# Optimization experiments

Hardware: AMD Instinct MI355X
Metric: run time of the kernel (lower is better)

The kernel has to match this reference:

```python
import jax, jax.numpy as jnp
import numpy as np

N_GRAPHS, NODES_PER, DEG, D = 128, 1024, 32, 256
N = N_GRAPHS * NODES_PER          # 131072 nodes
E = N * DEG                       # 4194304 edges
RATIO = 0.8
K = int(np.ceil(RATIO * NODES_PER))  # 820 nodes kept per graph


def setup_inputs() -> dict:
    key = jax.random.key(0)
    k1, k2, k3, k4 = jax.random.split(key, 4)
    x = jax.random.normal(k1, (N, D), dtype=jnp.float32)
    # intra-graph random edges: endpoints within [0, NODES_PER) + graph offset
    src = jax.random.randint(k2, (E,), 0, NODES_PER)
    dst = jax.random.randint(k3, (E,), 0, NODES_PER)
    goff = (jnp.arange(E) // (NODES_PER * DEG)) * NODES_PER
    edge_index = jnp.stack([src + goff, dst + goff]).astype(jnp.int32)
    batch = jnp.repeat(jnp.arange(N_GRAPHS, dtype=jnp.int32), NODES_PER)
    W = jax.random.normal(k4, (D, 1), dtype=jnp.float32) / np.sqrt(D)
    b = jnp.zeros((1,), dtype=jnp.float32)
    return {"x": x, "edge_index": edge_index, "batch": batch, "W": W, "b": b}


def _gcn_score(x, edge_index, W, b):
    # GCNConv(in_channels, 1) with added self-loops and symmetric normalization
    n = x.shape[0]
    row, col = edge_index[0], edge_index[1]  # source, target
    # degree at target, init 1.0 accounts for self-loop
    deg = jnp.ones((n,), x.dtype).at[col].add(jnp.ones_like(col, dtype=x.dtype))
    dinv = jax.lax.rsqrt(deg)
    h = x @ W                                 # [n, 1]
    norm = dinv[row] * dinv[col]              # [E]
    agg = jnp.zeros_like(h).at[col].add(norm[:, None] * h[row])
    agg = agg + (dinv * dinv)[:, None] * h    # self-loop contribution deg^-1 * h_i
    return (agg + b).squeeze(-1)              # [n]


def reference(x, edge_index, batch, W, b):
    score = _gcn_score(x, edge_index, W, b)                     # [N]
    # per-graph top-k (graphs are contiguous, equal size)
    score_g = score.reshape(N_GRAPHS, NODES_PER)
    _, idx = jax.lax.top_k(score_g, K)                          # [G, K]
    perm = (idx + jnp.arange(N_GRAPHS)[:, None] * NODES_PER).reshape(-1)  # [G*K]
    x_new = x[perm] * jnp.tanh(score[perm])[:, None]            # [G*K, D]
    batch_new = batch[perm]
    # filter_adj: remap kept nodes to new ids, mask edges with dropped endpoints
    new_id = jnp.full((x.shape[0],), -1, dtype=perm.dtype).at[perm].set(
        jnp.arange(perm.shape[0], dtype=perm.dtype))
    r2 = new_id[edge_index[0]]
    c2 = new_id[edge_index[1]]
    edge_mask = (r2 >= 0) & (c2 >= 0)                           # [E] valid edges
    edge_index_new = jnp.where(edge_mask, jnp.stack([r2, c2]), -1)  # [2, E], -1 = dropped
    return x_new, edge_index_new, edge_mask, batch_new, perm
```

## Files before the change

kernel.cpp:

```cpp
#include <hip/hip_runtime.h>
#include <math.h>

constexpr int NG    = 128;
constexpr int NP    = 1024;
constexpr int D     = 256;
constexpr int NTOT  = NG * NP;
constexpr int EPG   = NP * 32;
constexpr int ET    = NTOT * 32;
constexpr int KK    = 820;
constexpr int NKEEP = NG * KK;
constexpr int BPG   = 4;
constexpr int EPB   = EPG / BPG;
constexpr int NBE   = NG * BPG;

constexpr int K1_BLOCKS = 2048;
constexpr int K4_BLOCKS = 2048;
constexpr int K1_ROWS_PER_WAVE = NTOT / (K1_BLOCKS * 4);

constexpr long long OUT_X     = 0;
constexpr long long OUT_EI0   = (long long)NKEEP * D;
constexpr long long OUT_EI1   = OUT_EI0 + ET;
constexpr long long OUT_MASK  = OUT_EI0 + 2LL * ET;
constexpr long long OUT_BATCH = OUT_MASK + ET;
constexpr long long OUT_PERM  = OUT_BATCH + NKEEP;

__global__ __launch_bounds__(256) void k1_h_deg(const float* __restrict__ x,
                                                const float* __restrict__ W,
                                                const int* __restrict__ cols,
                                                float* __restrict__ h,
                                                int* __restrict__ new_id,
                                                int* __restrict__ deg_part) {
    __shared__ int cnt[NP];
    const int b    = blockIdx.x;
    const int t    = threadIdx.x;
    const int w    = t >> 6;
    const int lane = t & 63;
    const bool do_deg = (b < NBE);

    if (do_deg) {
        for (int i = t; i < NP; i += 256) cnt[i] = 0;
        __syncthreads();
    }

    float4 w4 = ((const float4*)W)[lane];
    const int base = (b * 4 + w) * K1_ROWS_PER_WAVE;
    for (int r = 0; r < K1_ROWS_PER_WAVE; ++r) {
        const int row = base + r;
        float4 a = ((const float4*)(x + (size_t)row * D))[lane];
        float s = a.x * w4.x + a.y * w4.y + a.z * w4.z + a.w * w4.w;
#pragma unroll
        for (int off = 32; off > 0; off >>= 1) s += __shfl_down(s, off, 64);
        if (lane == 0) { h[row] = s; new_id[row] = -1; }
    }

    if (do_deg) {
        const int g = b >> 2;
        const int4* c4 = (const int4*)(cols + (size_t)g * EPG + (size_t)(b & 3) * EPB);
#pragma unroll
        for (int i = t; i < EPB / 4; i += 256) {
            int4 c = c4[i];
            atomicAdd(&cnt[c.x & (NP - 1)], 1);
            atomicAdd(&cnt[c.y & (NP - 1)], 1);
            atomicAdd(&cnt[c.z & (NP - 1)], 1);
            atomicAdd(&cnt[c.w & (NP - 1)], 1);
        }
        __syncthreads();
        int* dst = deg_part + (size_t)b * NP;
        for (int i = t; i < NP; i += 256) dst[i] = cnt[i];
    }
}

__global__ __launch_bounds__(256) void k2_acc(const int* __restrict__ rows,
                                              const int* __restrict__ cols,
                                              const float* __restrict__ h,
                                              const int* __restrict__ deg_part,
                                              float* __restrict__ acc_part) {
    __shared__ float ul[NP];
    __shared__ float acc[NP];
    const int b = blockIdx.x;
    const int g = b >> 2;
    const int* dp = deg_part + (size_t)g * BPG * NP;
    for (int i = threadIdx.x; i < NP; i += 256) {
        int d = 1 + dp[i] + dp[NP + i] + dp[2 * NP + i] + dp[3 * NP + i];
        ul[i]  = rsqrtf((float)d) * h[g * NP + i];
        acc[i] = 0.0f;
    }
    __syncthreads();
    size_t eoff = (size_t)g * EPG + (size_t)(b & 3) * EPB;
    const int4* c4 = (const int4*)(cols + eoff);
    const int4* r4 = (const int4*)(rows + eoff);
#pragma unroll
    for (int i = threadIdx.x; i < EPB / 4; i += 256) {
        int4 c = c4[i];
        int4 r = r4[i];
        atomicAdd(&acc[c.x & (NP - 1)], ul[r.x & (NP - 1)]);
        atomicAdd(&acc[c.y & (NP - 1)], ul[r.y & (NP - 1)]);
        atomicAdd(&acc[c.z & (NP - 1)], ul[r.z & (NP - 1)]);
        atomicAdd(&acc[c.w & (NP - 1)], ul[r.w & (NP - 1)]);
    }
    __syncthreads();
    float* dst = acc_part + (size_t)b * NP;
    for (int i = threadIdx.x; i < NP; i += 256) dst[i] = acc[i];
}

__global__ __launch_bounds__(1024) void k3_sort(
        const float* __restrict__ h, const float* __restrict__ b,
        const int* __restrict__ deg_part, const float* __restrict__ acc_part,
        int* __restrict__ perm_i, int* __restrict__ new_id,
        float* __restrict__ factor,
        float* __restrict__ out_perm, float* __restrict__ out_batch) {
    __shared__ unsigned long long sk[NP];
    __shared__ float scl[NP];

    const int g = blockIdx.x;
    const int t = threadIdx.x;
    const int*   dp = deg_part + (size_t)g * BPG * NP;
    const float* ap = acc_part + (size_t)g * BPG * NP;

    int   d  = 1 + dp[t] + dp[NP + t] + dp[2 * NP + t] + dp[3 * NP + t];
    float av = ap[t] + ap[NP + t] + ap[2 * NP + t] + ap[3 * NP + t];
    float hv = h[g * NP + t];
    float di = rsqrtf((float)d);
    float score = di * av + di * di * hv + b[0];
    scl[t] = score;

    unsigned int fu = __float_as_uint(score);
    unsigned int s  = (fu & 0x80000000u) ? ~fu : (fu | 0x80000000u);
    unsigned long long key = ((unsigned long long)(~s) << 32) | (unsigned int)t;

    for (int k = 2; k <= NP; k <<= 1) {
        for (int j = k >> 1; j > 0; j >>= 1) {
            unsigned long long other;
            if (j < 64) {
                other = __shfl_xor(key, j, 64);
            } else {
                sk[t] = key;
                __syncthreads();
                other = sk[t ^ j];
                __syncthreads();
            }
            bool take_min = (((t & k) == 0) == ((t & j) == 0));
            bool omin = other < key;
            key = (take_min == omin) ? other : key;
        }
    }

    if (t < KK) {
        int idx  = (int)(key & 0xFFFFFFFFull);
        int node = g * NP + idx;
        int j    = g * KK + t;
        perm_i[j]    = node;
        new_id[node] = j;
        out_perm[j]  = (float)node;
        out_batch[j] = (float)g;
        factor[j]    = tanhf(scl[idx]);
    }
}

__global__ __launch_bounds__(256) void k4_gather_edge(
        const float* __restrict__ x,
        const int* __restrict__ rows, const int* __restrict__ cols,
        const int* __restrict__ new_id,
        const int* __restrict__ perm_i, const float* __restrict__ factor,
        float* __restrict__ out) {
    __shared__ int nid[NP];
    const int b    = blockIdx.x;
    const int t    = threadIdx.x;
    const int w    = t >> 6;
    const int lane = t & 63;

    if (b < NBE) {
        const int g = b >> 2;
        for (int i = t; i < NP; i += 256) nid[i] = new_id[g * NP + i];
        __syncthreads();
        size_t eoff = (size_t)g * EPG + (size_t)(b & 3) * EPB;
        const int4* r4 = (const int4*)(rows + eoff);
        const int4* c4 = (const int4*)(cols + eoff);
        float4* orr = (float4*)(out + OUT_EI0  + eoff);
        float4* occ = (float4*)(out + OUT_EI1  + eoff);
        float4* omm = (float4*)(out + OUT_MASK + eoff);
#pragma unroll
        for (int i = t; i < EPB / 4; i += 256) {
            int4 r = r4[i];
            int4 c = c4[i];
            float4 fr, fc, fm;
            {
                int nr = nid[r.x & (NP - 1)], nc = nid[c.x & (NP - 1)];
                bool m = (nr >= 0) && (nc >= 0);
                fr.x = m ? (float)nr : -1.0f; fc.x = m ? (float)nc : -1.0f; fm.x = m ? 1.0f : 0.0f;
            }
            {
                int nr = nid[r.y & (NP - 1)], nc = nid[c.y & (NP - 1)];
                bool m = (nr >= 0) && (nc >= 0);
                fr.y = m ? (float)nr : -1.0f; fc.y = m ? (float)nc : -1.0f; fm.y = m ? 1.0f : 0.0f;
            }
            {
                int nr = nid[r.z & (NP - 1)], nc = nid[c.z & (NP - 1)];
                bool m = (nr >= 0) && (nc >= 0);
                fr.z = m ? (float)nr : -1.0f; fc.z = m ? (float)nc : -1.0f; fm.z = m ? 1.0f : 0.0f;
            }
            {
                int nr = nid[r.w & (NP - 1)], nc = nid[c.w & (NP - 1)];
                bool m = (nr >= 0) && (nc >= 0);
                fr.w = m ? (float)nr : -1.0f; fc.w = m ? (float)nc : -1.0f; fm.w = m ? 1.0f : 0.0f;
            }
            orr[i] = fr;
            occ[i] = fc;
            omm[i] = fm;
        }
    }

    const int gw = b * 4 + w;
    for (int j = gw; j < NKEEP; j += K4_BLOCKS * 4) {
        const int node = perm_i[j];
        const float f  = factor[j];
        float4 v = ((const float4*)(x + (size_t)node * D))[lane];
        ((float4*)(out + OUT_X + (size_t)j * D))[lane] =
            make_float4(v.x * f, v.y * f, v.z * f, v.w * f);
    }
}

extern "C" void kernel_launch(void* const* d_in, const int* in_sizes, int n_in,
                              void* d_out, int out_size, void* d_ws, size_t ws_size,
                              hipStream_t stream) {
    (void)in_sizes; (void)n_in; (void)out_size; (void)ws_size;

    const float* x  = (const float*)d_in[0];
    const int*   ei = (const int*)d_in[1];
    const float* W  = (const float*)d_in[3];
    const float* b  = (const float*)d_in[4];
    float* out = (float*)d_out;

    float* wsf      = (float*)d_ws;
    float* h        = wsf;
    int*   new_id   = (int*)(wsf + NTOT);
    int*   perm_i   = (int*)(wsf + 2 * NTOT);
    float* factor   = wsf + 2 * NTOT + NKEEP;
    int*   deg_part = (int*)(wsf + 2 * NTOT + 2 * NKEEP);
    float* acc_part = wsf + 2 * NTOT + 2 * NKEEP + NBE * NP;

    const int* rows = ei;
    const int* cols = ei + ET;

    hipLaunchKernelGGL(k1_h_deg, dim3(K1_BLOCKS), dim3(256), 0, stream,
                       x, W, cols, h, new_id, deg_part);
    hipLaunchKernelGGL(k2_acc, dim3(NBE), dim3(256), 0, stream,
                       rows, cols, h, deg_part, acc_part);
    hipLaunchKernelGGL(k3_sort, dim3(NG), dim3(1024), 0, stream,
                       h, b, deg_part, acc_part, perm_i, new_id, factor,
                       out + OUT_PERM, out + OUT_BATCH);
    hipLaunchKernelGGL(k4_gather_edge, dim3(K4_BLOCKS), dim3(256), 0, stream,
                       x, rows, cols, new_id, perm_i, factor, out + OUT_X);
}
```

Baseline: 346.4 us.

## Fuse degree, aggregation and top-k sort into one per-graph kernel

Degree counting, edge aggregation and the bitonic top-k now run in a single 1024-thread block per graph, so the partial degree and accumulator arrays no longer make a round trip through global memory and one launch is dropped. The projection kernel processes 16 rows per wave with four independent reductions in flight. In the gather/edge kernel, edge blocks and row-gather blocks are split, and outputs use nontemporal stores. In exchange, the aggregation phase now runs on only 128 blocks, which may underuse the GPU, and each block reads its graph's edges twice.

```diff
diff --git a/kernel.cpp b/kernel.cpp
--- a/kernel.cpp
+++ b/kernel.cpp
@@ -14,8 +14,9 @@
 constexpr int NBE   = NG * BPG;
 
 constexpr int K1_BLOCKS = 2048;
-constexpr int K4_BLOCKS = 2048;
-constexpr int K1_ROWS_PER_WAVE = NTOT / (K1_BLOCKS * 4);
+constexpr int K3_BLOCKS = 2048;
+
+typedef float v4f __attribute__((ext_vector_type(4)));
 
 constexpr long long OUT_X     = 0;
 constexpr long long OUT_EI0   = (long long)NKEEP * D;
@@ -24,73 +25,83 @@
 constexpr long long OUT_BATCH = OUT_MASK + ET;
 constexpr long long OUT_PERM  = OUT_BATCH + NKEEP;
 
-__global__ __launch_bounds__(256) void k1_h_deg(const float* __restrict__ x,
-                                                const float* __restrict__ W,
-                                                const int* __restrict__ cols,
-                                                float* __restrict__ h,
-                                                int* __restrict__ new_id,
-                                                int* __restrict__ deg_part) {
-    __shared__ int cnt[NP];
-    const int b    = blockIdx.x;
+__global__ __launch_bounds__(256) void k1_h(const float* __restrict__ x,
+                                            const float* __restrict__ W,
+                                            float* __restrict__ h,
+                                            int* __restrict__ new_id) {
     const int t    = threadIdx.x;
     const int w    = t >> 6;
     const int lane = t & 63;
-    const bool do_deg = (b < NBE);
-
-    if (do_deg) {
-        for (int i = t; i < NP; i += 256) cnt[i] = 0;
-        __syncthreads();
-    }
+    const int gw   = blockIdx.x * 4 + w;
 
     float4 w4 = ((const float4*)W)[lane];
-    const int base = (b * 4 + w) * K1_ROWS_PER_WAVE;
-    for (int r = 0; r < K1_ROWS_PER_WAVE; ++r) {
-        const int row = base + r;
-        float4 a = ((const float4*)(x + (size_t)row * D))[lane];
-        float s = a.x * w4.x + a.y * w4.y + a.z * w4.z + a.w * w4.w;
-#pragma unroll
-        for (int off = 32; off > 0; off >>= 1) s += __shfl_down(s, off, 64);
-        if (lane == 0) { h[row] = s; new_id[row] = -1; }
-    }
-
-    if (do_deg) {
-        const int g = b >> 2;
-        const int4* c4 = (const int4*)(cols + (size_t)g * EPG + (size_t)(b & 3) * EPB);
-#pragma unroll
-        for (int i = t; i < EPB / 4; i += 256) {
-            int4 c = c4[i];
-            atomicAdd(&cnt[c.x & (NP - 1)], 1);
-            atomicAdd(&cnt[c.y & (NP - 1)], 1);
-            atomicAdd(&cnt[c.z & (NP - 1)], 1);
-            atomicAdd(&cnt[c.w & (NP - 1)], 1);
-        }
-        __syncthreads();
-        int* dst = deg_part + (size_t)b * NP;
-        for (int i = t; i < NP; i += 256) dst[i] = cnt[i];
-    }
-}
-
-__global__ __launch_bounds__(256) void k2_acc(const int* __restrict__ rows,
-                                              const int* __restrict__ cols,
-                                              const float* __restrict__ h,
-                                              const int* __restrict__ deg_part,
-                                              float* __restrict__ acc_part) {
-    __shared__ float ul[NP];
+    const float4* xp = (const float4*)(x + (size_t)gw * 16 * D);
+
+#pragma unroll
+    for (int c = 0; c < 4; ++c) {
+        float4 a0 = xp[(c * 4 + 0) * 64 + lane];
+        float4 a1 = xp[(c * 4 + 1) * 64 + lane];
+        float4 a2 = xp[(c * 4 + 2) * 64 + lane];
+        float4 a3 = xp[(c * 4 + 3) * 64 + lane];
+        float s0 = a0.x * w4.x + a0.y * w4.y + a0.z * w4.z + a0.w * w4.w;
+        float s1 = a1.x * w4.x + a1.y * w4.y + a1.z * w4.z + a1.w * w4.w;
+        float s2 = a2.x * w4.x + a2.y * w4.y + a2.z * w4.z + a2.w * w4.w;
+        float s3 = a3.x * w4.x + a3.y * w4.y + a3.z * w4.z + a3.w * w4.w;
+#pragma unroll
+        for (int off = 32; off > 0; off >>= 1) {
+            s0 += __shfl_down(s0, off, 64);
+            s1 += __shfl_down(s1, off, 64);
+            s2 += __shfl_down(s2, off, 64);
+            s3 += __shfl_down(s3, off, 64);
+        }
+        if (lane == 0) {
+            const int r = gw * 16 + c * 4;
+            h[r] = s0; h[r + 1] = s1; h[r + 2] = s2; h[r + 3] = s3;
+            new_id[r]     = -1; new_id[r + 1] = -1;
+            new_id[r + 2] = -1; new_id[r + 3] = -1;
+        }
+    }
+}
+
+__global__ __launch_bounds__(1024) void k2_graph(
+        const float* __restrict__ h,  const float* __restrict__ bptr,
+        const int* __restrict__ rows, const int* __restrict__ cols,
+        int* __restrict__ perm_i,     int* __restrict__ new_id,
+        float* __restrict__ factor,
+        float* __restrict__ out_perm, float* __restrict__ out_batch) {
+    __shared__ unsigned long long sk[NP];
     __shared__ float acc[NP];
-    const int b = blockIdx.x;
-    const int g = b >> 2;
-    const int* dp = deg_part + (size_t)g * BPG * NP;
-    for (int i = threadIdx.x; i < NP; i += 256) {
-        int d = 1 + dp[i] + dp[NP + i] + dp[2 * NP + i] + dp[3 * NP + i];
-        ul[i]  = rsqrtf((float)d) * h[g * NP + i];
-        acc[i] = 0.0f;
-    }
-    __syncthreads();
-    size_t eoff = (size_t)g * EPG + (size_t)(b & 3) * EPB;
-    const int4* c4 = (const int4*)(cols + eoff);
-    const int4* r4 = (const int4*)(rows + eoff);
-#pragma unroll
-    for (int i = threadIdx.x; i < EPB / 4; i += 256) {
+    __shared__ float scl[NP];
+    int*   cnt = (int*)sk;
+    float* ul  = (float*)sk + NP;
+
+    const int g = blockIdx.x;
+    const int t = threadIdx.x;
+
+    const float hv = h[g * NP + t];
+    cnt[t] = 0;
+    __syncthreads();
+
+    const int4* c4 = (const int4*)(cols + (size_t)g * EPG);
+    const int4* r4 = (const int4*)(rows + (size_t)g * EPG);
+
+#pragma unroll
+    for (int i = t; i < EPG / 4; i += 1024) {
+        int4 c = c4[i];
+        atomicAdd(&cnt[c.x & (NP - 1)], 1);
+        atomicAdd(&cnt[c.y & (NP - 1)], 1);
+        atomicAdd(&cnt[c.z & (NP - 1)], 1);
+        atomicAdd(&cnt[c.w & (NP - 1)], 1);
+    }
+    __syncthreads();
+
+    const float di = rsqrtf((float)(1 + cnt[t]));
+    ul[t]  = di * hv;
+    acc[t] = 0.0f;
+    __syncthreads();
+
+#pragma unroll
+    for (int i = t; i < EPG / 4; i += 1024) {
         int4 c = c4[i];
         int4 r = r4[i];
         atomicAdd(&acc[c.x & (NP - 1)], ul[r.x & (NP - 1)]);
@@ -99,29 +110,8 @@
         atomicAdd(&acc[c.w & (NP - 1)], ul[r.w & (NP - 1)]);
     }
     __syncthreads();
-    float* dst = acc_part + (size_t)b * NP;
-    for (int i = threadIdx.x; i < NP; i += 256) dst[i] = acc[i];
-}
-
-__global__ __launch_bounds__(1024) void k3_sort(
-        const float* __restrict__ h, const float* __restrict__ b,
-        const int* __restrict__ deg_part, const float* __restrict__ acc_part,
-        int* __restrict__ perm_i, int* __restrict__ new_id,
-        float* __restrict__ factor,
-        float* __restrict__ out_perm, float* __restrict__ out_batch) {
-    __shared__ unsigned long long sk[NP];
-    __shared__ float scl[NP];
-
-    const int g = blockIdx.x;
-    const int t = threadIdx.x;
-    const int*   dp = deg_part + (size_t)g * BPG * NP;
-    const float* ap = acc_part + (size_t)g * BPG * NP;
-
-    int   d  = 1 + dp[t] + dp[NP + t] + dp[2 * NP + t] + dp[3 * NP + t];
-    float av = ap[t] + ap[NP + t] + ap[2 * NP + t] + ap[3 * NP + t];
-    float hv = h[g * NP + t];
-    float di = rsqrtf((float)d);
-    float score = di * av + di * di * hv + b[0];
+
+    const float score = di * acc[t] + di * di * hv + bptr[0];
     scl[t] = score;
 
     unsigned int fu = __float_as_uint(score);
@@ -157,7 +147,7 @@
     }
 }
 
-__global__ __launch_bounds__(256) void k4_gather_edge(
+__global__ __launch_bounds__(256) void k3_gather_edge(
         const float* __restrict__ x,
         const int* __restrict__ rows, const int* __restrict__ cols,
         const int* __restrict__ new_id,
@@ -176,14 +166,14 @@
         size_t eoff = (size_t)g * EPG + (size_t)(b & 3) * EPB;
         const int4* r4 = (const int4*)(rows + eoff);
         const int4* c4 = (const int4*)(cols + eoff);
-        float4* orr = (float4*)(out + OUT_EI0  + eoff);
-        float4* occ = (float4*)(out + OUT_EI1  + eoff);
-        float4* omm = (float4*)(out + OUT_MASK + eoff);
+        v4f* orr = (v4f*)(out + OUT_EI0  + eoff);
+        v4f* occ = (v4f*)(out + OUT_EI1  + eoff);
+        v4f* omm = (v4f*)(out + OUT_MASK + eoff);
 #pragma unroll
         for (int i = t; i < EPB / 4; i += 256) {
             int4 r = r4[i];
             int4 c = c4[i];
-            float4 fr, fc, fm;
+            v4f fr, fc, fm;
             {
                 int nr = nid[r.x & (NP - 1)], nc = nid[c.x & (NP - 1)];
                 bool m = (nr >= 0) && (nc >= 0);
@@ -204,19 +194,20 @@
                 bool m = (nr >= 0) && (nc >= 0);
                 fr.w = m ? (float)nr : -1.0f; fc.w = m ? (float)nc : -1.0f; fm.w = m ? 1.0f : 0.0f;
             }
-            orr[i] = fr;
-            occ[i] = fc;
-            omm[i] = fm;
-        }
-    }
-
-    const int gw = b * 4 + w;
-    for (int j = gw; j < NKEEP; j += K4_BLOCKS * 4) {
-        const int node = perm_i[j];
-        const float f  = factor[j];
-        float4 v = ((const float4*)(x + (size_t)node * D))[lane];
-        ((float4*)(out + OUT_X + (size_t)j * D))[lane] =
-            make_float4(v.x * f, v.y * f, v.z * f, v.w * f);
+            __builtin_nontemporal_store(fr, &orr[i]);
+            __builtin_nontemporal_store(fc, &occ[i]);
+            __builtin_nontemporal_store(fm, &omm[i]);
+        }
+    } else {
+        const int gw = (b - NBE) * 4 + w;
+        for (int j = gw; j < NKEEP; j += (K3_BLOCKS - NBE) * 4) {
+            const int node = perm_i[j];
+            const float f  = factor[j];
+            float4 v = ((const float4*)(x + (size_t)node * D))[lane];
+            v4f o;
+            o.x = v.x * f; o.y = v.y * f; o.z = v.z * f; o.w = v.w * f;
+            __builtin_nontemporal_store(o, &((v4f*)(out + OUT_X + (size_t)j * D))[lane]);
+        }
     }
 }
 
@@ -236,19 +227,15 @@
     int*   new_id   = (int*)(wsf + NTOT);
     int*   perm_i   = (int*)(wsf + 2 * NTOT);
     float* factor   = wsf + 2 * NTOT + NKEEP;
-    int*   deg_part = (int*)(wsf + 2 * NTOT + 2 * NKEEP);
-    float* acc_part = wsf + 2 * NTOT + 2 * NKEEP + NBE * NP;
 
     const int* rows = ei;
     const int* cols = ei + ET;
 
-    hipLaunchKernelGGL(k1_h_deg, dim3(K1_BLOCKS), dim3(256), 0, stream,
-                       x, W, cols, h, new_id, deg_part);
-    hipLaunchKernelGGL(k2_acc, dim3(NBE), dim3(256), 0, stream,
-                       rows, cols, h, deg_part, acc_part);
-    hipLaunchKernelGGL(k3_sort, dim3(NG), dim3(1024), 0, stream,
-                       h, b, deg_part, acc_part, perm_i, new_id, factor,
+    hipLaunchKernelGGL(k1_h, dim3(K1_BLOCKS), dim3(256), 0, stream,
+                       x, W, h, new_id);
+    hipLaunchKernelGGL(k2_graph, dim3(NG), dim3(1024), 0, stream,
+                       h, b, rows, cols, perm_i, new_id, factor,
                        out + OUT_PERM, out + OUT_BATCH);
-    hipLaunchKernelGGL(k4_gather_edge, dim3(K4_BLOCKS), dim3(256), 0, stream,
-                       x, rows, cols, new_id, perm_i, factor, out + OUT_X);
-}
+    hipLaunchKernelGGL(k3_gather_edge, dim3(K3_BLOCKS), dim3(256), 0, stream,
+                       x, rows, cols, new_id, perm_i, factor, out);
+}
```

Measured after the change: 350.5 us. About the same (+1.2%).
